# Kernel tuning notes

Measured on AMD Instinct MI355X. Metric: run time of the kernel, lower is better.

The kernel has to match this reference:

```python
import jax, jax.numpy as jnp
import numpy as np

B, N, IN_DIM, D, H, NC = 4, 1024, 8, 128, 8, 64
DK = D // H      # per-head key/value dim = 16
FF = 512         # hard-coded feedforward hidden
N_ENC = 6        # encoder layers


def _u(key, shape):
    s = 1.0 / np.sqrt(shape[-1])
    return jax.random.uniform(key, shape, jnp.float32, -s, s)


def setup_inputs() -> dict:
    key = jax.random.key(0)
    ks = jax.random.split(key, 24)
    inp = {}
    inp["node_inputs"] = jax.random.normal(ks[0], (B, N, IN_DIM), jnp.float32)
    inp["node_padding_mask"] = jnp.zeros((B, 1, N), jnp.int32)
    inp["edge_mask"] = jax.random.randint(ks[1], (B, N, N), 0, 2).astype(jnp.int32)
    inp["center_mask"] = jnp.zeros((B, 1, NC), jnp.int32)
    inp["center_index"] = jax.random.randint(ks[2], (B, 1, NC), 0, N)
    inp["target_index"] = jax.random.randint(ks[3], (B, 1, 1), 0, N)
    inp["current_index"] = jax.random.randint(ks[4], (B, 1, 1), 0, N)
    inp["edge_inputs"] = jax.random.randint(ks[5], (B, N, 20), 0, N)
    # params
    inp["init_W"] = _u(ks[6], (IN_DIM, D)); inp["init_b"] = jnp.zeros((D,), jnp.float32)
    inp["enc_wq"] = _u(ks[7], (N_ENC, H, D, DK))
    inp["enc_wk"] = _u(ks[8], (N_ENC, H, D, DK))
    inp["enc_wv"] = _u(ks[9], (N_ENC, H, D, DK))
    inp["enc_wo"] = _u(ks[10], (N_ENC, H, DK, D))
    inp["enc_ln1_g"] = jnp.ones((N_ENC, D), jnp.float32); inp["enc_ln1_b"] = jnp.zeros((N_ENC, D), jnp.float32)
    inp["enc_w1"] = _u(ks[11], (N_ENC, D, FF)); inp["enc_b1"] = jnp.zeros((N_ENC, FF), jnp.float32)
    inp["enc_w2"] = _u(ks[12], (N_ENC, FF, D)); inp["enc_b2"] = jnp.zeros((N_ENC, D), jnp.float32)
    inp["enc_ln2_g"] = jnp.ones((N_ENC, D), jnp.float32); inp["enc_ln2_b"] = jnp.zeros((N_ENC, D), jnp.float32)
    inp["dec_wq"] = _u(ks[13], (H, D, DK))
    inp["dec_wk"] = _u(ks[14], (H, D, DK))
    inp["dec_wv"] = _u(ks[15], (H, D, DK))
    inp["dec_wo"] = _u(ks[16], (H, DK, D))
    inp["dec_ln1_g"] = jnp.ones((D,), jnp.float32); inp["dec_ln1_b"] = jnp.zeros((D,), jnp.float32)
    inp["dec_w1"] = _u(ks[17], (D, FF)); inp["dec_b1"] = jnp.zeros((FF,), jnp.float32)
    inp["dec_w2"] = _u(ks[18], (FF, D)); inp["dec_b2"] = jnp.zeros((D,), jnp.float32)
    inp["dec_ln2_g"] = jnp.ones((D,), jnp.float32); inp["dec_ln2_b"] = jnp.zeros((D,), jnp.float32)
    inp["tgt_W"] = _u(ks[19], (2 * D, D)); inp["tgt_b"] = jnp.zeros((D,), jnp.float32)
    inp["ptr_wq"] = _u(ks[20], (D, D))
    inp["ptr_wk"] = _u(ks[21], (D, D))
    return inp


def _ln(x, g, b):
    m = jnp.mean(x, -1, keepdims=True)
    v = jnp.mean((x - m) ** 2, -1, keepdims=True)
    return (x - m) * jax.lax.rsqrt(v + 1e-5) * g + b


def _mha(q, k, v, wq, wk, wv, wo, mask):
    # per-head projections exactly as the torch module: [H, B, n, DK]
    Q = jnp.einsum('bqd,hde->hbqe', q, wq)
    K = jnp.einsum('bkd,hde->hbke', k, wk)
    V = jnp.einsum('bkd,hde->hbke', v, wv)
    U = jnp.einsum('hbqe,hbke->hbqk', Q, K) * (1.0 / np.sqrt(DK))
    if mask is not None:
        U = jnp.where(mask[None] > 0, -1e8, U)
    A = jax.nn.softmax(U, axis=-1)
    Hd = jnp.einsum('hbqk,hbke->hbqe', A, V)
    out = jnp.einsum('hbqe,hed->bqd', Hd, wo)
    return out, A


def _gather(x, idx):
    # x [B, N, D], idx [B, M, 1] -> [B, M, D]  (torch.gather with repeat)
    return jnp.take_along_axis(x, jnp.broadcast_to(idx, (x.shape[0], idx.shape[1], x.shape[2])), axis=1)


def reference(node_inputs, node_padding_mask, edge_mask, center_mask, center_index,
              target_index, current_index, edge_inputs,
              init_W, init_b,
              enc_wq, enc_wk, enc_wv, enc_wo, enc_ln1_g, enc_ln1_b,
              enc_w1, enc_b1, enc_w2, enc_b2, enc_ln2_g, enc_ln2_b,
              dec_wq, dec_wk, dec_wv, dec_wo, dec_ln1_g, dec_ln1_b,
              dec_w1, dec_b1, dec_w2, dec_b2, dec_ln2_g, dec_ln2_b,
              tgt_W, tgt_b, ptr_wq, ptr_wk):
    x = node_inputs @ init_W + init_b                      # initial_embedding
    enc_mask = edge_mask + node_padding_mask               # attn_mask + key_padding_mask, [B,N,N]
    for i in range(N_ENC):                                 # Encoder, 6 layers
        h = _ln(x, enc_ln1_g[i], enc_ln1_b[i])
        a, _ = _mha(h, h, h, enc_wq[i], enc_wk[i], enc_wv[i], enc_wo[i], enc_mask)
        h = a + x
        f = _ln(h, enc_ln2_g[i], enc_ln2_b[i])
        f = jax.nn.relu(f @ enc_w1[i] + enc_b1[i]) @ enc_w2[i] + enc_b2[i]
        x = f + h
    enh = x                                                # enhanced_node_feature [B,N,D]
    ci = jnp.transpose(center_index, (0, 2, 1))            # [B,NC,1]
    tgt_f = _gather(enh, target_index)                     # [B,1,D]
    cur_f = _gather(enh, current_index)                    # [B,1,D]
    cen_f = _gather(enh, ci)                               # [B,NC,D]
    # target_decoder (1 DecoderLayer; normalization1 applied to tgt AND memory)
    tgt_n = _ln(tgt_f, dec_ln1_g, dec_ln1_b)
    mem_n = _ln(enh, dec_ln1_g, dec_ln1_b)
    a, _ = _mha(tgt_n, mem_n, mem_n, dec_wq, dec_wk, dec_wv, dec_wo, node_padding_mask)
    h = a + tgt_f
    f = _ln(h, dec_ln2_g, dec_ln2_b)
    f = jax.nn.relu(f @ dec_w1 + dec_b1) @ dec_w2 + dec_b2
    enh_tgt = f + h                                        # [B,1,D]
    emb_tgt = jnp.concatenate([enh_tgt, tgt_f], -1) @ tgt_W + tgt_b
    # pointer1 (SingleHeadAttention, key_dim = D, tanh clipping 10)
    Q = emb_tgt @ ptr_wq                                   # [B,1,D]
    K = cen_f @ ptr_wk                                     # [B,NC,D]
    U = jnp.einsum('bqd,bkd->bqk', Q, K) * (1.0 / np.sqrt(D))
    U = 10.0 * jnp.tanh(U)
    U = jnp.where(center_mask == 1, -1e8, U)
    center_logp = jax.nn.log_softmax(U, axis=-1)[:, 0, :]  # [B,NC]
    idx = jnp.argmax(center_logp, axis=1)
    bidx = jnp.arange(B)
    selected_center_index = ci[bidx, idx, :]               # [B,1]
    selected_center_feature = cen_f[bidx, idx, :][:, None, :]  # [B,1,D]
    return (enh, cur_f, selected_center_index, selected_center_feature, center_logp, cen_f)
```

## Files before the change

kernel.cpp:

```cpp
#include <hip/hip_runtime.h>

constexpr int kB = 4, kN = 1024, kIn = 8, kD = 128, kH = 8, kNC = 64,
              kDK = 16, kFF = 512, kEnc = 6, kR = kB * kN;

__device__ __forceinline__ float wredsum(float v) {
  v += __shfl_xor(v, 1);  v += __shfl_xor(v, 2);  v += __shfl_xor(v, 4);
  v += __shfl_xor(v, 8);  v += __shfl_xor(v, 16); v += __shfl_xor(v, 32);
  return v;
}
__device__ __forceinline__ float wredmax(float v) {
  v = fmaxf(v, __shfl_xor(v, 1));  v = fmaxf(v, __shfl_xor(v, 2));
  v = fmaxf(v, __shfl_xor(v, 4));  v = fmaxf(v, __shfl_xor(v, 8));
  v = fmaxf(v, __shfl_xor(v, 16)); v = fmaxf(v, __shfl_xor(v, 32));
  return v;
}
__device__ __forceinline__ float red4(float v) {
  v += __shfl_xor(v, 1);  v += __shfl_xor(v, 2);
  return v;
}


__global__ __launch_bounds__(256) void repack_qkv(
    const float* __restrict__ wq, const float* __restrict__ wk,
    const float* __restrict__ wv, float* __restrict__ out, int layers) {
  int i = blockIdx.x * 256 + threadIdx.x;
  if (i >= layers * kD * kD) return;
  int l = i / (kD * kD);
  int rem = i - l * kD * kD;
  int d = rem >> 7;
  int c = rem & 127;
  int src = ((l * kH + (c >> 4)) * kD + d) * kDK + (c & 15);
  out[(size_t)(l * 3 + 0) * 16384 + rem] = wq[src];
  out[(size_t)(l * 3 + 1) * 16384 + rem] = wk[src];
  out[(size_t)(l * 3 + 2) * 16384 + rem] = wv[src];
}

__global__ __launch_bounds__(256) void pack_mask(
    const int* __restrict__ edge_mask, const int* __restrict__ pad_mask,
    unsigned long long* __restrict__ bits_t) {
  int row = blockIdx.x;
  int b = row / kN;
  int q = row % kN;
  int lane = threadIdx.x & 63;
  int wv = threadIdx.x >> 6;
  for (int c0 = wv; c0 < 16; c0 += 4) {
    int k = c0 * 64 + lane;
    int m = edge_mask[(size_t)row * kN + k] + pad_mask[b * kN + k];
    unsigned long long bal = __ballot(m > 0);
    if (lane == 0) bits_t[((size_t)b * 16 + c0) * kN + q] = bal;
  }
}

__global__ __launch_bounds__(256) void pack_pad(
    const int* __restrict__ pad_mask, unsigned long long* __restrict__ bits) {
  int b = blockIdx.x;
  int lane = threadIdx.x & 63;
  int wv = threadIdx.x >> 6;
  for (int c0 = wv; c0 < 16; c0 += 4) {
    int k = c0 * 64 + lane;
    unsigned long long bal = __ballot(pad_mask[b * kN + k] > 0);
    if (lane == 0) bits[b * 16 + c0] = bal;
  }
}

__global__ __launch_bounds__(256) void init_proj(
    const float* __restrict__ ni, const float* __restrict__ W,
    const float* __restrict__ bias, float* __restrict__ x) {
  int i = blockIdx.x * 256 + threadIdx.x;
  int r = i >> 7, c = i & 127;
  float acc = bias[c];
#pragma unroll
  for (int k = 0; k < kIn; k++) acc = fmaf(ni[r * kIn + k], W[k * kD + c], acc);
  x[i] = acc;
}

template <int K, int LN, int RELU, int MODE>
__global__ __launch_bounds__(256) void gtile4(
    const float* __restrict__ A, const float* __restrict__ Wg,
    const float* __restrict__ gamma, const float* __restrict__ beta,
    const float* __restrict__ bias, const float* __restrict__ resid,
    float* __restrict__ O0, float* __restrict__ O1, float* __restrict__ O2,
    int Cfull) {
  constexpr int NC = K / 32;
  __shared__ float As[16][K + 4];
  __shared__ float Ws[2][32][128];
  int r0 = blockIdx.x * 16;
  int y = blockIdx.y;
  const float* Wb;
  int wstride;
  if constexpr (MODE == 2) { Wb = Wg + (size_t)y * K * 128; wstride = 128; }
  else { Wb = Wg + (size_t)y * 128; wstride = Cfull; }

  if constexpr (LN) {
    static_assert(K == 128, "LN requires K==128");
    int w = threadIdx.x >> 6, lane = threadIdx.x & 63;
#pragma unroll
    for (int i = 0; i < 4; i++) {
      int rr = w * 4 + i;
      const float* xr = A + (size_t)(r0 + rr) * 128;
      float2 v = *(const float2*)(xr + lane * 2);
      float mean = wredsum(v.x + v.y) * (1.0f / 128.f);
      float dx = v.x - mean, dy = v.y - mean;
      float var = wredsum(dx * dx + dy * dy) * (1.0f / 128.f);
      float rstd = rsqrtf(var + 1e-5f);
      int c = lane * 2;
      As[rr][c] = dx * rstd * gamma[c] + beta[c];
      As[rr][c + 1] = dy * rstd * gamma[c + 1] + beta[c + 1];
    }
  } else {
    constexpr int NF4 = K / 4;
    for (int f = threadIdx.x; f < 16 * NF4; f += 256) {
      int row = f / NF4, c4i = f % NF4;
      *(float4*)&As[row][c4i * 4] =
          *(const float4*)(A + (size_t)(r0 + row) * K + c4i * 4);
    }
  }

  int wrow = threadIdx.x >> 5;
  int wc4 = threadIdx.x & 31;
  float4 wreg[4];
  auto loadW = [&](int kc) {
    const float* Wr = Wb + (size_t)(kc * 32 + wrow) * wstride + wc4 * 4;
#pragma unroll
    for (int j = 0; j < 4; j++)
      wreg[j] = *(const float4*)(Wr + (size_t)8 * j * wstride);
  };
  auto writeW = [&](int buf) {
#pragma unroll
    for (int j = 0; j < 4; j++)
      *(float4*)&Ws[buf][wrow + 8 * j][wc4 * 4] = wreg[j];
  };

  loadW(0);
  writeW(0);

  int c4 = (threadIdx.x & 31) * 4;
  int rg = threadIdx.x >> 5;
  float acc[2][4] = {};
  for (int kc = 0; kc < NC; kc++) {
    if (kc + 1 < NC) loadW(kc + 1);
    __syncthreads();
#pragma unroll
    for (int k4 = 0; k4 < 8; k4++) {
      float4 a0 = *(const float4*)&As[rg * 2][kc * 32 + k4 * 4];
      float4 a1 = *(const float4*)&As[rg * 2 + 1][kc * 32 + k4 * 4];
#pragma unroll
      for (int m = 0; m < 4; m++) {
        float4 wv = *(const float4*)&Ws[kc & 1][k4 * 4 + m][c4];
        float av0 = ((const float*)&a0)[m];
        float av1 = ((const float*)&a1)[m];
        acc[0][0] = fmaf(av0, wv.x, acc[0][0]);
        acc[0][1] = fmaf(av0, wv.y, acc[0][1]);
        acc[0][2] = fmaf(av0, wv.z, acc[0][2]);
        acc[0][3] = fmaf(av0, wv.w, acc[0][3]);
        acc[1][0] = fmaf(av1, wv.x, acc[1][0]);
        acc[1][1] = fmaf(av1, wv.y, acc[1][1]);
        acc[1][2] = fmaf(av1, wv.z, acc[1][2]);
        acc[1][3] = fmaf(av1, wv.w, acc[1][3]);
      }
    }
    if (kc + 1 < NC) writeW((kc + 1) & 1);
  }

#pragma unroll
  for (int rr = 0; rr < 2; rr++) {
    int r = r0 + rg * 2 + rr;
    if constexpr (MODE == 2) {
#pragma unroll
      for (int j = 0; j < 4; j++) {
        int c = c4 + j;
        float v = acc[rr][j];
        int hh = c >> 4, e = c & 15;
        int bb = r >> 10, n = r & 1023;
        float* P = (y == 0) ? O0 : (y == 1) ? O1 : O2;
        P[(((size_t)(bb * kH + hh)) * kN + n) * kDK + e] = v;
      }
    } else {
      int colg = y * 128 + c4;
      float4 v = make_float4(acc[rr][0], acc[rr][1], acc[rr][2], acc[rr][3]);
      if (bias) {
        float4 bv = *(const float4*)(bias + colg);
        v.x += bv.x; v.y += bv.y; v.z += bv.z; v.w += bv.w;
      }
      if (resid) {
        float4 rv = *(const float4*)(resid + (size_t)r * Cfull + colg);
        v.x += rv.x; v.y += rv.y; v.z += rv.z; v.w += rv.w;
      }
      if (RELU) {
        v.x = fmaxf(v.x, 0.f); v.y = fmaxf(v.y, 0.f);
        v.z = fmaxf(v.z, 0.f); v.w = fmaxf(v.w, 0.f);
      }
      *(float4*)(O0 + (size_t)r * Cfull + colg) = v;
    }
  }
}

__global__ __launch_bounds__(512) void attn_flash3(
    const float* __restrict__ Q, const float* __restrict__ K,
    const float* __restrict__ V, const unsigned long long* __restrict__ bits_t,
    float* __restrict__ Hd) {
  __shared__ float Ks[8][64][20];
  __shared__ float Vs[8][64][20];
  int bh = blockIdx.x, qt = blockIdx.y;
  int b = bh >> 3, h = bh & 7;
  int w = threadIdx.x >> 6, lane = threadIdx.x & 63;
  int q0 = qt * 128 + lane, q1 = q0 + 64;
  const float4* qp0 = (const float4*)(Q + ((size_t)bh * kN + q0) * kDK);
  const float4* qp1 = (const float4*)(Q + ((size_t)bh * kN + q1) * kDK);
  float4 qa0 = qp0[0], qa1 = qp0[1], qa2 = qp0[2], qa3 = qp0[3];
  float4 qb0 = qp1[0], qb1 = qp1[1], qb2 = qp1[2], qb3 = qp1[3];
  const float* Kb = K + (size_t)bh * kN * kDK;
  const float* Vb = V + (size_t)bh * kN * kDK;
  float mx0 = -3.0e38f, l0 = 0.f, mx1 = -3.0e38f, l1 = 0.f;
  float acc0[16], acc1[16];
#pragma unroll
  for (int e = 0; e < 16; e++) { acc0[e] = 0.f; acc1[e] = 0.f; }
  for (int t = 0; t < 2; t++) {
    int kk = w * 128 + t * 64 + lane;
    const float4* kp = (const float4*)(Kb + (size_t)kk * kDK);
    float4 ka = kp[0], kb2 = kp[1], kc = kp[2], kd = kp[3];
    const float4* vp = (const float4*)(Vb + (size_t)kk * kDK);
    float4 va = vp[0], vb = vp[1], vc = vp[2], vd = vp[3];
    unsigned long long mb0 = bits_t[((size_t)b * 16 + w * 2 + t) * kN + q0];
    unsigned long long mb1 = bits_t[((size_t)b * 16 + w * 2 + t) * kN + q1];
    ((float4*)&Ks[w][lane][0])[0] = ka;  ((float4*)&Ks[w][lane][0])[1] = kb2;
    ((float4*)&Ks[w][lane][0])[2] = kc;  ((float4*)&Ks[w][lane][0])[3] = kd;
    ((float4*)&Vs[w][lane][0])[0] = va;  ((float4*)&Vs[w][lane][0])[1] = vb;
    ((float4*)&Vs[w][lane][0])[2] = vc;  ((float4*)&Vs[w][lane][0])[3] = vd;
#pragma unroll 2
    for (int k2 = 0; k2 < 64; k2++) {
      const float4* kr = (const float4*)&Ks[w][k2][0];
      float4 k0 = kr[0], k1 = kr[1], k2v = kr[2], k3 = kr[3];
      float s0 = qa0.x * k0.x + qa0.y * k0.y + qa0.z * k0.z + qa0.w * k0.w
               + qa1.x * k1.x + qa1.y * k1.y + qa1.z * k1.z + qa1.w * k1.w
               + qa2.x * k2v.x + qa2.y * k2v.y + qa2.z * k2v.z + qa2.w * k2v.w
               + qa3.x * k3.x + qa3.y * k3.y + qa3.z * k3.z + qa3.w * k3.w;
      float s1 = qb0.x * k0.x + qb0.y * k0.y + qb0.z * k0.z + qb0.w * k0.w
               + qb1.x * k1.x + qb1.y * k1.y + qb1.z * k1.z + qb1.w * k1.w
               + qb2.x * k2v.x + qb2.y * k2v.y + qb2.z * k2v.z + qb2.w * k2v.w
               + qb3.x * k3.x + qb3.y * k3.y + qb3.z * k3.z + qb3.w * k3.w;
      s0 *= 0.25f; s1 *= 0.25f;
      if ((mb0 >> k2) & 1ull) s0 = -1e8f;
      if ((mb1 >> k2) & 1ull) s1 = -1e8f;
      float d0 = s0 - mx0;
      if (d0 > 8.f) {
        float sc = __expf(-d0);
        l0 *= sc;
#pragma unroll
        for (int e = 0; e < 16; e++) acc0[e] *= sc;
        mx0 = s0; d0 = 0.f;
      }
      float p0 = __expf(d0);
      l0 += p0;
      float d1 = s1 - mx1;
      if (d1 > 8.f) {
        float sc = __expf(-d1);
        l1 *= sc;
#pragma unroll
        for (int e = 0; e < 16; e++) acc1[e] *= sc;
        mx1 = s1; d1 = 0.f;
      }
      float p1 = __expf(d1);
      l1 += p1;
      const float4* vr = (const float4*)&Vs[w][k2][0];
      float4 v0 = vr[0], v1 = vr[1], v2 = vr[2], v3 = vr[3];
      acc0[0] = fmaf(p0, v0.x, acc0[0]);   acc0[1] = fmaf(p0, v0.y, acc0[1]);
      acc0[2] = fmaf(p0, v0.z, acc0[2]);   acc0[3] = fmaf(p0, v0.w, acc0[3]);
      acc0[4] = fmaf(p0, v1.x, acc0[4]);   acc0[5] = fmaf(p0, v1.y, acc0[5]);
      acc0[6] = fmaf(p0, v1.z, acc0[6]);   acc0[7] = fmaf(p0, v1.w, acc0[7]);
      acc0[8] = fmaf(p0, v2.x, acc0[8]);   acc0[9] = fmaf(p0, v2.y, acc0[9]);
      acc0[10] = fmaf(p0, v2.z, acc0[10]); acc0[11] = fmaf(p0, v2.w, acc0[11]);
      acc0[12] = fmaf(p0, v3.x, acc0[12]); acc0[13] = fmaf(p0, v3.y, acc0[13]);
      acc0[14] = fmaf(p0, v3.z, acc0[14]); acc0[15] = fmaf(p0, v3.w, acc0[15]);
      acc1[0] = fmaf(p1, v0.x, acc1[0]);   acc1[1] = fmaf(p1, v0.y, acc1[1]);
      acc1[2] = fmaf(p1, v0.z, acc1[2]);   acc1[3] = fmaf(p1, v0.w, acc1[3]);
      acc1[4] = fmaf(p1, v1.x, acc1[4]);   acc1[5] = fmaf(p1, v1.y, acc1[5]);
      acc1[6] = fmaf(p1, v1.z, acc1[6]);   acc1[7] = fmaf(p1, v1.w, acc1[7]);
      acc1[8] = fmaf(p1, v2.x, acc1[8]);   acc1[9] = fmaf(p1, v2.y, acc1[9]);
      acc1[10] = fmaf(p1, v2.z, acc1[10]); acc1[11] = fmaf(p1, v2.w, acc1[11]);
      acc1[12] = fmaf(p1, v3.x, acc1[12]); acc1[13] = fmaf(p1, v3.y, acc1[13]);
      acc1[14] = fmaf(p1, v3.z, acc1[14]); acc1[15] = fmaf(p1, v3.w, acc1[15]);
    }
  }
  __syncthreads();
  float* M0 = &Ks[w][lane][0];
  float* M1 = &Vs[w][lane][0];
#pragma unroll
  for (int e = 0; e < 16; e++) { M0[e] = acc0[e]; M1[e] = acc1[e]; }
  M0[16] = mx0; M0[17] = l0;
  M1[16] = mx1; M1[17] = l1;
  __syncthreads();
#pragma unroll
  for (int half = 0; half < 2; half++) {
    const float* M = half ? &Vs[0][0][0] : &Ks[0][0][0];
    float mv[8];
#pragma unroll
    for (int p = 0; p < 8; p++) mv[p] = M[(p * 64 + lane) * 20 + 16];
    float mstar = mv[0];
#pragma unroll
    for (int p = 1; p < 8; p++) mstar = fmaxf(mstar, mv[p]);
    float f[8];
    float L = 0.f;
#pragma unroll
    for (int p = 0; p < 8; p++) {
      f[p] = __expf(mv[p] - mstar);
      L += f[p] * M[(p * 64 + lane) * 20 + 17];
    }
    float invL = 1.0f / L;
    float o[2];
#pragma unroll
    for (int e = 0; e < 2; e++) {
      int ei = w * 2 + e;
      float a = 0.f;
#pragma unroll
      for (int p = 0; p < 8; p++) a += f[p] * M[(p * 64 + lane) * 20 + ei];
      o[e] = a * invL;
    }
    int q = qt * 128 + half * 64 + lane;
    *(float2*)(Hd + ((size_t)(b * kN + q)) * kD + h * kDK + w * 2) =
        make_float2(o[0], o[1]);
  }
}


__global__ __launch_bounds__(256) void dec_prep(
    const float* __restrict__ enh, const int* __restrict__ tgt_idx,
    const int* __restrict__ cur_idx, const int* __restrict__ cen_idx,
    const float* __restrict__ Wq,
    const float* __restrict__ ln1_g, const float* __restrict__ ln1_b,
    const float* __restrict__ dec_wk,
    float* __restrict__ out_curf, float* __restrict__ out_cenf,
    float* __restrict__ tgtf_ws, float* __restrict__ qk_ws) {
  __shared__ float tgtf_s[128], tgtn[128], qd[128];
  int b = blockIdx.x, t = threadIdx.x;
  int lane = t & 63, w = t >> 6;
  int ti = tgt_idx[b], cui = cur_idx[b];
  if (t < 128) {
    float tf = enh[((size_t)b * kN + ti) * kD + t];
    tgtf_s[t] = tf;
    tgtf_ws[b * kD + t] = tf;
    out_curf[b * kD + t] = enh[((size_t)b * kN + cui) * kD + t];
  }
  for (int i = t; i < kNC * kD; i += 256) {
    int c = i >> 7, e = i & 127;
    out_cenf[((size_t)b * kNC + c) * kD + e] =
        enh[((size_t)b * kN + cen_idx[b * kNC + c]) * kD + e];
  }
  __syncthreads();
  if (w == 0) {
    float vx = tgtf_s[lane * 2], vy = tgtf_s[lane * 2 + 1];
    float mean = wredsum(vx + vy) * (1.0f / 128.f);
    float dx = vx - mean, dy = vy - mean;
    float var = wredsum(dx * dx + dy * dy) * (1.0f / 128.f);
    float rstd = rsqrtf(var + 1e-5f);
    tgtn[lane * 2] = dx * rstd * ln1_g[lane * 2] + ln1_b[lane * 2];
    tgtn[lane * 2 + 1] = dy * rstd * ln1_g[lane * 2 + 1] + ln1_b[lane * 2 + 1];
  }
  __syncthreads();
  if (t < 128) {
    float a = 0.f;
#pragma unroll 8
    for (int k = 0; k < 128; k++) a = fmaf(tgtn[k], Wq[k * 128 + t], a);
    qd[t] = a;
  }
  __syncthreads();
  int h = t >> 5, d0 = (t & 31) * 4;
#pragma unroll
  for (int j = 0; j < 4; j++) {
    int d = d0 + j;
    const float4* wp = (const float4*)(dec_wk + (((size_t)h * 128 + d) << 4));
    float a = 0.f;
#pragma unroll
    for (int r = 0; r < 4; r++) {
      float4 wv = wp[r];
      a += wv.x * qd[h * 16 + r * 4] + wv.y * qd[h * 16 + r * 4 + 1] +
           wv.z * qd[h * 16 + r * 4 + 2] + wv.w * qd[h * 16 + r * 4 + 3];
    }
    qk_ws[b * 1024 + h * 128 + d] = 0.25f * a;
  }
}

__global__ __launch_bounds__(256) void dec_score(
    const float* __restrict__ enh, const float* __restrict__ ln_g,
    const float* __restrict__ ln_b, const float* __restrict__ qk_ws,
    const unsigned long long* __restrict__ padbits,
    float* __restrict__ ln_ws, float* __restrict__ scores) {
  __shared__ float qs[8][128];
  int b = blockIdx.x, nt = blockIdx.y, t = threadIdx.x;
  for (int i = t; i < 1024; i += 256) ((float*)qs)[i] = qk_ws[b * 1024 + i];
  __syncthreads();
  int w = t >> 6, lane = t & 63, ri = lane >> 2, q4 = lane & 3;
  int n = nt * 64 + w * 16 + ri;
  const float* row = enh + ((size_t)b * kN + n) * kD;
  float4 xv[8];
#pragma unroll
  for (int j = 0; j < 8; j++) xv[j] = *(const float4*)(row + j * 16 + q4 * 4);
  float s1 = 0.f;
#pragma unroll
  for (int j = 0; j < 8; j++) s1 += xv[j].x + xv[j].y + xv[j].z + xv[j].w;
  s1 = red4(s1);
  float mean = s1 * (1.0f / 128.f);
  float s2 = 0.f;
#pragma unroll
  for (int j = 0; j < 8; j++) {
    xv[j].x -= mean; xv[j].y -= mean; xv[j].z -= mean; xv[j].w -= mean;
    s2 += xv[j].x * xv[j].x + xv[j].y * xv[j].y + xv[j].z * xv[j].z +
          xv[j].w * xv[j].w;
  }
  s2 = red4(s2);
  float rstd = rsqrtf(s2 * (1.0f / 128.f) + 1e-5f);
#pragma unroll
  for (int j = 0; j < 8; j++) {
    int d0 = j * 16 + q4 * 4;
    float4 g = *(const float4*)(ln_g + d0);
    float4 be = *(const float4*)(ln_b + d0);
    xv[j].x = xv[j].x * rstd * g.x + be.x;
    xv[j].y = xv[j].y * rstd * g.y + be.y;
    xv[j].z = xv[j].z * rstd * g.z + be.z;
    xv[j].w = xv[j].w * rstd * g.w + be.w;
    *(float4*)(ln_ws + ((size_t)b * kN + n) * kD + d0) = xv[j];
  }
  bool mk = (padbits[b * 16 + (n >> 6)] >> (n & 63)) & 1ull;
#pragma unroll
  for (int h = 0; h < 8; h++) {
    float p = 0.f;
#pragma unroll
    for (int j = 0; j < 8; j++) {
      float4 qv = *(const float4*)&qs[h][j * 16 + q4 * 4];
      p += xv[j].x * qv.x + xv[j].y * qv.y + xv[j].z * qv.z + xv[j].w * qv.w;
    }
    p = red4(p);
    if (q4 == 0) scores[((size_t)b * 8 + h) * 1024 + n] = mk ? -1e8f : p;
  }
}

__global__ __launch_bounds__(256) void dec_softmax(
    const float* __restrict__ scores, float* __restrict__ ml) {
  int b = blockIdx.x, t = threadIdx.x, w = t >> 6, lane = t & 63;
  for (int hi = 0; hi < 2; hi++) {
    int h = w + hi * 4;
    const float* sr = scores + ((size_t)b * 8 + h) * 1024;
    float v[16];
    float m = -3.0e38f;
#pragma unroll
    for (int i = 0; i < 16; i++) { v[i] = sr[i * 64 + lane]; m = fmaxf(m, v[i]); }
    m = wredmax(m);
    float l = 0.f;
#pragma unroll
    for (int i = 0; i < 16; i++) l += __expf(v[i] - m);
    l = wredsum(l);
    if (lane == 0) { ml[(b * 8 + h) * 2] = m; ml[(b * 8 + h) * 2 + 1] = l; }
  }
}

__global__ __launch_bounds__(256) void dec_attnsum(
    const float* __restrict__ ln_ws, const float* __restrict__ scores,
    const float* __restrict__ ml, float* __restrict__ partial) {
  __shared__ float lns[64][128];
  __shared__ float ps[8][64];
  int b = blockIdx.x, nt = blockIdx.y, t = threadIdx.x;
  for (int i = t; i < 64 * 32; i += 256) {
    int nn = i >> 5, c4 = i & 31;
    *(float4*)&lns[nn][c4 * 4] =
        *(const float4*)(ln_ws + ((size_t)b * kN + nt * 64 + nn) * kD + c4 * 4);
  }
  for (int i = t; i < 512; i += 256) {
    int h = i >> 6, nn = i & 63;
    float m = ml[(b * 8 + h) * 2], l = ml[(b * 8 + h) * 2 + 1];
    ps[h][nn] =
        __expf(scores[((size_t)b * 8 + h) * 1024 + nt * 64 + nn] - m) / l;
  }
  __syncthreads();
  int h = t >> 5, d0 = (t & 31) * 4;
  float4 acc = make_float4(0.f, 0.f, 0.f, 0.f);
  for (int nn = 0; nn < 64; nn++) {
    float p = ps[h][nn];
    float4 lv = *(const float4*)&lns[nn][d0];
    acc.x = fmaf(p, lv.x, acc.x); acc.y = fmaf(p, lv.y, acc.y);
    acc.z = fmaf(p, lv.z, acc.z); acc.w = fmaf(p, lv.w, acc.w);
  }
  *(float4*)(partial + ((size_t)(b * 16 + nt) * 8 + h) * 128 + d0) = acc;
}

__global__ __launch_bounds__(1024) void dec_tail(
    const float* __restrict__ partial, const float* __restrict__ dec_wv,
    const float* __restrict__ dwo, const float* __restrict__ tgtf_ws,
    const float* __restrict__ cenf_g, const float* __restrict__ Kp,
    const int* __restrict__ cen_idx, const int* __restrict__ center_mask,
    const float* __restrict__ ln2_g, const float* __restrict__ ln2_b,
    const float* __restrict__ w1, const float* __restrict__ b1,
    const float* __restrict__ w2, const float* __restrict__ b2,
    const float* __restrict__ tgt_W, const float* __restrict__ tgt_b,
    const float* __restrict__ ptr_wq,
    float* __restrict__ out_selidx, float* __restrict__ out_selfeat,
    float* __restrict__ out_logp) {
  __shared__ float wsum[8][132];
  __shared__ float red[8][132];
  __shared__ float red2[2][520];
  __shared__ float red16[16][68];
  __shared__ float tgtf[128], hdd[128], dechs[128], decfs[128], dects[512],
                   embs[128], qps[128];
  __shared__ int bi_s;
  int b = blockIdx.x, t = threadIdx.x;
  int c = t & 127, p = t >> 7;
  int lane = t & 63, w = t >> 6;

  {
    float a = 0.f;
#pragma unroll
    for (int tt = 0; tt < 16; tt++)
      a += partial[((size_t)(b * 16 + tt) * 8 + p) * 128 + c];
    wsum[p][c] = a;
    if (t < 128) tgtf[t] = tgtf_ws[b * kD + t];
  }
  __syncthreads();

  {
    int h = c >> 4, e = c & 15;
    float a = 0.f;
#pragma unroll
    for (int i = 0; i < 16; i++) {
      int d = p * 16 + i;
      a = fmaf(wsum[h][d], dec_wv[((size_t)h * 128 + d) * 16 + e], a);
    }
    red[p][c] = a;
  }
  __syncthreads();
  if (t < 128) {
    float a = 0.f;
#pragma unroll
    for (int q = 0; q < 8; q++) a += red[q][t];
    hdd[t] = a;
  }
  __syncthreads();

  {
    float a = 0.f;
#pragma unroll
    for (int i = 0; i < 16; i++) {
      int k = p * 16 + i;
      a = fmaf(hdd[k], dwo[k * 128 + c], a);
    }
    red[p][c] = a;
  }
  __syncthreads();
  if (t < 128) {
    float a = 0.f;
#pragma unroll
    for (int q = 0; q < 8; q++) a += red[q][t];
    dechs[t] = a + tgtf[t];
  }
  __syncthreads();

  if (w == 0) {
    float vx = dechs[lane * 2], vy = dechs[lane * 2 + 1];
    float mean = wredsum(vx + vy) * (1.0f / 128.f);
    float dx = vx - mean, dy = vy - mean;
    float var = wredsum(dx * dx + dy * dy) * (1.0f / 128.f);
    float rstd = rsqrtf(var + 1e-5f);
    decfs[lane * 2] = dx * rstd * ln2_g[lane * 2] + ln2_b[lane * 2];
    decfs[lane * 2 + 1] = dy * rstd * ln2_g[lane * 2 + 1] + ln2_b[lane * 2 + 1];
  }
  __syncthreads();

  {
    int c5 = t & 511, p2 = t >> 9;
    float a = 0.f;
#pragma unroll 8
    for (int i = 0; i < 64; i++) {
      int k = p2 * 64 + i;
      a = fmaf(decfs[k], w1[k * 512 + c5], a);
    }
    red2[p2][c5] = a;
  }
  __syncthreads();
  if (t < 512) dects[t] = fmaxf(red2[0][t] + red2[1][t] + b1[t], 0.f);
  __syncthreads();

  {
    float a = 0.f;
#pragma unroll 8
    for (int i = 0; i < 64; i++) {
      int k = p * 64 + i;
      a = fmaf(dects[k], w2[k * 128 + c], a);
    }
    red[p][c] = a;
  }
  __syncthreads();
  if (t < 128) {
    float a = 0.f;
#pragma unroll
    for (int q = 0; q < 8; q++) a += red[q][t];
    decfs[t] = a + b2[t] + dechs[t];
  }
  __syncthreads();

  {
    float a = 0.f;
#pragma unroll
    for (int i = 0; i < 32; i++) {
      int k = p * 32 + i;
      float vkk = (k < 128) ? decfs[k] : tgtf[k - 128];
      a = fmaf(vkk, tgt_W[k * 128 + c], a);
    }
    red[p][c] = a;
  }
  __syncthreads();
  if (t < 128) {
    float a = 0.f;
#pragma unroll
    for (int q = 0; q < 8; q++) a += red[q][t];
    embs[t] = a + tgt_b[t];
  }
  __syncthreads();

  {
    float a = 0.f;
#pragma unroll
    for (int i = 0; i < 16; i++) {
      int k = p * 16 + i;
      a = fmaf(embs[k], ptr_wq[k * 128 + c], a);
    }
    red[p][c] = a;
  }
  __syncthreads();
  if (t < 128) {
    float a = 0.f;
#pragma unroll
    for (int q = 0; q < 8; q++) a += red[q][t];
    qps[t] = a;
  }
  __syncthreads();

  {
    int cen = t & 63, p16 = t >> 6;
    float a = 0.f;
#pragma unroll
    for (int i = 0; i < 8; i++) {
      int k = p16 * 8 + i;
      a = fmaf(qps[k], Kp[((size_t)(b * kNC + cen)) * kD + k], a);
    }
    red16[p16][cen] = a;
  }
  __syncthreads();
  if (w == 0) {
    float u = 0.f;
#pragma unroll
    for (int q = 0; q < 16; q++) u += red16[q][lane];
    u *= 0.08838834764831845f;
    u = 10.0f * tanhf(u);
    if (center_mask[b * kNC + lane] == 1) u = -1e8f;
    float m = wredmax(u);
    float ex = __expf(u - m);
    float sum = wredsum(ex);
    out_logp[b * kNC + lane] = u - m - logf(sum);
    float bm = u; int bi = lane;
#pragma unroll
    for (int o = 32; o; o >>= 1) {
      float om = __shfl_xor(bm, o);
      int oi = __shfl_xor(bi, o);
      if (om > bm || (om == bm && oi < bi)) { bm = om; bi = oi; }
    }
    if (lane == 0) {
      out_selidx[b] = (float)cen_idx[b * kNC + bi];
      bi_s = bi;
    }
  }
  __syncthreads();
  if (t < 128)
    out_selfeat[b * kD + t] = cenf_g[((size_t)(b * kNC + bi_s)) * kD + t];
}


extern "C" void kernel_launch(void* const* d_in, const int* in_sizes, int n_in,
                              void* d_out, int out_size, void* d_ws,
                              size_t ws_size, hipStream_t stream) {
  (void)in_sizes; (void)n_in; (void)out_size; (void)ws_size;
  const float* node_inputs = (const float*)d_in[0];
  const int* pad_mask = (const int*)d_in[1];
  const int* edge_mask = (const int*)d_in[2];
  const int* center_mask = (const int*)d_in[3];
  const int* center_index = (const int*)d_in[4];
  const int* target_index = (const int*)d_in[5];
  const int* current_index = (const int*)d_in[6];
  const float* init_W = (const float*)d_in[8];
  const float* init_b = (const float*)d_in[9];
  const float* enc_wq = (const float*)d_in[10];
  const float* enc_wk = (const float*)d_in[11];
  const float* enc_wv = (const float*)d_in[12];
  const float* enc_wo = (const float*)d_in[13];
  const float* enc_ln1_g = (const float*)d_in[14];
  const float* enc_ln1_b = (const float*)d_in[15];
  const float* enc_w1 = (const float*)d_in[16];
  const float* enc_b1 = (const float*)d_in[17];
  const float* enc_w2 = (const float*)d_in[18];
  const float* enc_b2 = (const float*)d_in[19];
  const float* enc_ln2_g = (const float*)d_in[20];
  const float* enc_ln2_b = (const float*)d_in[21];
  const float* dec_wq = (const float*)d_in[22];
  const float* dec_wk = (const float*)d_in[23];
  const float* dec_wv = (const float*)d_in[24];
  const float* dec_wo = (const float*)d_in[25];
  const float* dec_ln1_g = (const float*)d_in[26];
  const float* dec_ln1_b = (const float*)d_in[27];
  const float* dec_w1 = (const float*)d_in[28];
  const float* dec_b1 = (const float*)d_in[29];
  const float* dec_w2 = (const float*)d_in[30];
  const float* dec_b2 = (const float*)d_in[31];
  const float* dec_ln2_g = (const float*)d_in[32];
  const float* dec_ln2_b = (const float*)d_in[33];
  const float* tgt_W = (const float*)d_in[34];
  const float* tgt_b = (const float*)d_in[35];
  const float* ptr_wq = (const float*)d_in[36];
  const float* ptr_wk = (const float*)d_in[37];

  float* out_enh = (float*)d_out;
  float* out_curf = out_enh + kB * kN * kD;
  float* out_selidx = out_curf + kB * kD;
  float* out_selfeat = out_selidx + kB;
  float* out_logp = out_selfeat + kB * kD;
  float* out_cenf = out_logp + kB * kNC;

  char* wsp = (char*)d_ws;
  size_t off = 0;
  auto alloc = [&](size_t n) {
    char* p = wsp + off;
    off = (off + n + 255) & ~(size_t)255;
    return p;
  };
  float* x   = (float*)alloc(kR * kD * 4);
  float* h2  = (float*)alloc(kR * kD * 4);
  float* Qb  = (float*)alloc(kR * kD * 4);
  float* Kb  = (float*)alloc(kR * kD * 4);
  float* Vb  = (float*)alloc(kR * kD * 4);
  float* Hd  = (float*)alloc(kR * kD * 4);
  float* tb  = (float*)alloc(kR * kFF * 4);
  unsigned long long* bits_t  = (unsigned long long*)alloc(kR * 16 * 8);
  unsigned long long* padbits = (unsigned long long*)alloc(kB * 16 * 8);
  float* ewqkv = (float*)alloc(kEnc * 3 * kD * kD * 4);
  float* dqkvW = (float*)alloc(3 * kD * kD * 4);
  float* ln_ws = (float*)alloc(kR * kD * 4);
  float* scores_ws = (float*)alloc(kB * kH * kN * 4);
  float* ml_ws = (float*)alloc(kB * kH * 2 * 4);
  float* partial_ws = (float*)alloc(kB * 16 * kH * kD * 4);
  float* qk_ws = (float*)alloc(kB * kH * kD * 4);
  float* tgtf_ws = (float*)alloc(kB * kD * 4);
  float* Kp_ws = (float*)alloc(kB * kNC * kD * 4);

  repack_qkv<<<(kEnc * kD * kD + 255) / 256, 256, 0, stream>>>(
      enc_wq, enc_wk, enc_wv, ewqkv, kEnc);
  repack_qkv<<<(kD * kD + 255) / 256, 256, 0, stream>>>(
      dec_wq, dec_wk, dec_wv, dqkvW, 1);
  pack_mask<<<kB * kN, 256, 0, stream>>>(edge_mask, pad_mask, bits_t);
  pack_pad<<<kB, 256, 0, stream>>>(pad_mask, padbits);
  init_proj<<<kR * kD / 256, 256, 0, stream>>>(node_inputs, init_W, init_b, x);

  for (int l = 0; l < kEnc; l++) {
    const float* wo_l = enc_wo + (size_t)l * kH * kDK * kD;
    gtile4<128, 1, 0, 2><<<dim3(kR / 16, 3), 256, 0, stream>>>(
        x, ewqkv + (size_t)l * 3 * kD * kD, enc_ln1_g + l * kD,
        enc_ln1_b + l * kD, nullptr, nullptr, Qb, Kb, Vb, kD);
    attn_flash3<<<dim3(kB * kH, kN / 128), 512, 0, stream>>>(Qb, Kb, Vb,
                                                             bits_t, Hd);
    gtile4<128, 0, 0, 0><<<dim3(kR / 16, 1), 256, 0, stream>>>(
        Hd, wo_l, nullptr, nullptr, nullptr, x, h2, nullptr, nullptr, kD);
    gtile4<128, 1, 1, 0><<<dim3(kR / 16, kFF / 128), 256, 0, stream>>>(
        h2, enc_w1 + (size_t)l * kD * kFF, enc_ln2_g + l * kD,
        enc_ln2_b + l * kD, enc_b1 + l * kFF, nullptr, tb, nullptr, nullptr, kFF);
    float* xout = (l == kEnc - 1) ? out_enh : x;
    gtile4<512, 0, 0, 0><<<dim3(kR / 16, 1), 256, 0, stream>>>(
        tb, enc_w2 + (size_t)l * kFF * kD, nullptr, nullptr, enc_b2 + l * kD,
        h2, xout, nullptr, nullptr, kD);
  }

  dec_prep<<<kB, 256, 0, stream>>>(out_enh, target_index, current_index,
                                   center_index, dqkvW, dec_ln1_g, dec_ln1_b,
                                   dec_wk, out_curf, out_cenf, tgtf_ws, qk_ws);
  gtile4<128, 0, 0, 0><<<dim3(kB * kNC / 16, 1), 256, 0, stream>>>(
      out_cenf, ptr_wk, nullptr, nullptr, nullptr, nullptr, Kp_ws, nullptr,
      nullptr, kD);
  dec_score<<<dim3(kB, 16), 256, 0, stream>>>(out_enh, dec_ln1_g, dec_ln1_b,
                                              qk_ws, padbits, ln_ws, scores_ws);
  dec_softmax<<<kB, 256, 0, stream>>>(scores_ws, ml_ws);
  dec_attnsum<<<dim3(kB, 16), 256, 0, stream>>>(ln_ws, scores_ws, ml_ws,
                                                partial_ws);
  dec_tail<<<kB, 1024, 0, stream>>>(
      partial_ws, dec_wv, dec_wo, tgtf_ws, out_cenf, Kp_ws, center_index,
      center_mask, dec_ln2_g, dec_ln2_b, dec_w1, dec_b1, dec_w2, dec_b2,
      tgt_W, tgt_b, ptr_wq, out_selidx, out_selfeat, out_logp);
}
```

Before: 797.9 us.

## Split encoder attention over key halves with four queries per thread and merge

Replaces the single-pass flash attention kernel with a split-K version. Each block handles 256 queries against one half of the keys, and each thread keeps four queries in registers so every K/V row read from shared memory is reused four times. Partial max, sum and accumulators go to a workspace, and a separate merge kernel combines the two halves. This raises per-thread register pressure, adds a global round trip for partials plus an extra launch per layer, and serializes the intra-block reduction over four syncs.

```diff
diff --git a/kernel.cpp b/kernel.cpp
--- a/kernel.cpp
+++ b/kernel.cpp
@@ -195,131 +195,141 @@
   }
 }
 
-__global__ __launch_bounds__(512) void attn_flash3(
+__global__ __launch_bounds__(512) void attn_part(
     const float* __restrict__ Q, const float* __restrict__ K,
     const float* __restrict__ V, const unsigned long long* __restrict__ bits_t,
-    float* __restrict__ Hd) {
+    float* __restrict__ part) {
   __shared__ float Ks[8][64][20];
   __shared__ float Vs[8][64][20];
-  int bh = blockIdx.x, qt = blockIdx.y;
+  int bh = blockIdx.x, qt = blockIdx.y, ks = blockIdx.z;
+  int b = bh >> 3;
+  int w = threadIdx.x >> 6, lane = threadIdx.x & 63;
+  int qbase = qt * 256 + lane;
+  float4 qr[4][4];
+#pragma unroll
+  for (int i = 0; i < 4; i++) {
+    const float4* qp = (const float4*)(Q + ((size_t)bh * kN + qbase + i * 64) * kDK);
+    qr[i][0] = qp[0]; qr[i][1] = qp[1]; qr[i][2] = qp[2]; qr[i][3] = qp[3];
+  }
+  int kk = ks * 512 + w * 64 + lane;
+  {
+    const float4* kp = (const float4*)(K + ((size_t)bh * kN + kk) * kDK);
+    const float4* vp = (const float4*)(V + ((size_t)bh * kN + kk) * kDK);
+    ((float4*)&Ks[w][lane][0])[0] = kp[0]; ((float4*)&Ks[w][lane][0])[1] = kp[1];
+    ((float4*)&Ks[w][lane][0])[2] = kp[2]; ((float4*)&Ks[w][lane][0])[3] = kp[3];
+    ((float4*)&Vs[w][lane][0])[0] = vp[0]; ((float4*)&Vs[w][lane][0])[1] = vp[1];
+    ((float4*)&Vs[w][lane][0])[2] = vp[2]; ((float4*)&Vs[w][lane][0])[3] = vp[3];
+  }
+  int tile = ks * 8 + w;
+  unsigned long long mb[4];
+#pragma unroll
+  for (int i = 0; i < 4; i++)
+    mb[i] = bits_t[((size_t)b * 16 + tile) * kN + qbase + i * 64];
+
+  float mx[4], lsum[4], acc[4][16];
+#pragma unroll
+  for (int i = 0; i < 4; i++) {
+    mx[i] = -3.0e38f; lsum[i] = 0.f;
+#pragma unroll
+    for (int e = 0; e < 16; e++) acc[i][e] = 0.f;
+  }
+
+#pragma unroll 2
+  for (int k2 = 0; k2 < 64; k2++) {
+    const float4* kr = (const float4*)&Ks[w][k2][0];
+    float4 k0 = kr[0], k1 = kr[1], k2v = kr[2], k3 = kr[3];
+    const float4* vr = (const float4*)&Vs[w][k2][0];
+    float4 v0 = vr[0], v1 = vr[1], v2 = vr[2], v3 = vr[3];
+#pragma unroll
+    for (int i = 0; i < 4; i++) {
+      float s = qr[i][0].x * k0.x + qr[i][0].y * k0.y + qr[i][0].z * k0.z +
+                qr[i][0].w * k0.w + qr[i][1].x * k1.x + qr[i][1].y * k1.y +
+                qr[i][1].z * k1.z + qr[i][1].w * k1.w + qr[i][2].x * k2v.x +
+                qr[i][2].y * k2v.y + qr[i][2].z * k2v.z + qr[i][2].w * k2v.w +
+                qr[i][3].x * k3.x + qr[i][3].y * k3.y + qr[i][3].z * k3.z +
+                qr[i][3].w * k3.w;
+      s *= 0.25f;
+      if ((mb[i] >> k2) & 1ull) s = -1e8f;
+      float d = s - mx[i];
+      if (d > 8.f) {
+        float sc = __expf(-d);
+        lsum[i] *= sc;
+#pragma unroll
+        for (int e = 0; e < 16; e++) acc[i][e] *= sc;
+        mx[i] = s; d = 0.f;
+      }
+      float p = __expf(d);
+      lsum[i] += p;
+      acc[i][0] = fmaf(p, v0.x, acc[i][0]);
+      acc[i][1] = fmaf(p, v0.y, acc[i][1]);
+      acc[i][2] = fmaf(p, v0.z, acc[i][2]);
+      acc[i][3] = fmaf(p, v0.w, acc[i][3]);
+      acc[i][4] = fmaf(p, v1.x, acc[i][4]);
+      acc[i][5] = fmaf(p, v1.y, acc[i][5]);
+      acc[i][6] = fmaf(p, v1.z, acc[i][6]);
+      acc[i][7] = fmaf(p, v1.w, acc[i][7]);
+      acc[i][8] = fmaf(p, v2.x, acc[i][8]);
+      acc[i][9] = fmaf(p, v2.y, acc[i][9]);
+      acc[i][10] = fmaf(p, v2.z, acc[i][10]);
+      acc[i][11] = fmaf(p, v2.w, acc[i][11]);
+      acc[i][12] = fmaf(p, v3.x, acc[i][12]);
+      acc[i][13] = fmaf(p, v3.y, acc[i][13]);
+      acc[i][14] = fmaf(p, v3.z, acc[i][14]);
+      acc[i][15] = fmaf(p, v3.w, acc[i][15]);
+    }
+  }
+  __syncthreads();
+  for (int i = 0; i < 4; i++) {
+    float* dst = &Ks[w][lane][0];
+#pragma unroll
+    for (int e = 0; e < 16; e++) dst[e] = acc[i][e];
+    dst[16] = mx[i];
+    dst[17] = lsum[i];
+    __syncthreads();
+    if (w == 0) {
+      float mv[8];
+#pragma unroll
+      for (int p = 0; p < 8; p++) mv[p] = Ks[p][lane][16];
+      float mstar = mv[0];
+#pragma unroll
+      for (int p = 1; p < 8; p++) mstar = fmaxf(mstar, mv[p]);
+      float f[8];
+      float L = 0.f;
+#pragma unroll
+      for (int p = 0; p < 8; p++) {
+        f[p] = __expf(mv[p] - mstar);
+        L += f[p] * Ks[p][lane][17];
+      }
+      int q = qt * 256 + i * 64 + lane;
+      float* op = part + ((size_t)(ks * 32 + bh) * kN + q) * 20;
+#pragma unroll
+      for (int e = 0; e < 16; e++) {
+        float a = 0.f;
+#pragma unroll
+        for (int p = 0; p < 8; p++) a += f[p] * Ks[p][lane][e];
+        op[e] = a;
+      }
+      op[16] = mstar;
+      op[17] = L;
+    }
+    __syncthreads();
+  }
+}
+
+__global__ __launch_bounds__(256) void attn_merge(
+    const float* __restrict__ part, float* __restrict__ Hd) {
+  int idx = blockIdx.x * 256 + threadIdx.x;
+  int bh = idx >> 10, q = idx & 1023;
   int b = bh >> 3, h = bh & 7;
-  int w = threadIdx.x >> 6, lane = threadIdx.x & 63;
-  int q0 = qt * 128 + lane, q1 = q0 + 64;
-  const float4* qp0 = (const float4*)(Q + ((size_t)bh * kN + q0) * kDK);
-  const float4* qp1 = (const float4*)(Q + ((size_t)bh * kN + q1) * kDK);
-  float4 qa0 = qp0[0], qa1 = qp0[1], qa2 = qp0[2], qa3 = qp0[3];
-  float4 qb0 = qp1[0], qb1 = qp1[1], qb2 = qp1[2], qb3 = qp1[3];
-  const float* Kb = K + (size_t)bh * kN * kDK;
-  const float* Vb = V + (size_t)bh * kN * kDK;
-  float mx0 = -3.0e38f, l0 = 0.f, mx1 = -3.0e38f, l1 = 0.f;
-  float acc0[16], acc1[16];
-#pragma unroll
-  for (int e = 0; e < 16; e++) { acc0[e] = 0.f; acc1[e] = 0.f; }
-  for (int t = 0; t < 2; t++) {
-    int kk = w * 128 + t * 64 + lane;
-    const float4* kp = (const float4*)(Kb + (size_t)kk * kDK);
-    float4 ka = kp[0], kb2 = kp[1], kc = kp[2], kd = kp[3];
-    const float4* vp = (const float4*)(Vb + (size_t)kk * kDK);
-    float4 va = vp[0], vb = vp[1], vc = vp[2], vd = vp[3];
-    unsigned long long mb0 = bits_t[((size_t)b * 16 + w * 2 + t) * kN + q0];
-    unsigned long long mb1 = bits_t[((size_t)b * 16 + w * 2 + t) * kN + q1];
-    ((float4*)&Ks[w][lane][0])[0] = ka;  ((float4*)&Ks[w][lane][0])[1] = kb2;
-    ((float4*)&Ks[w][lane][0])[2] = kc;  ((float4*)&Ks[w][lane][0])[3] = kd;
-    ((float4*)&Vs[w][lane][0])[0] = va;  ((float4*)&Vs[w][lane][0])[1] = vb;
-    ((float4*)&Vs[w][lane][0])[2] = vc;  ((float4*)&Vs[w][lane][0])[3] = vd;
-#pragma unroll 2
-    for (int k2 = 0; k2 < 64; k2++) {
-      const float4* kr = (const float4*)&Ks[w][k2][0];
-      float4 k0 = kr[0], k1 = kr[1], k2v = kr[2], k3 = kr[3];
-      float s0 = qa0.x * k0.x + qa0.y * k0.y + qa0.z * k0.z + qa0.w * k0.w
-               + qa1.x * k1.x + qa1.y * k1.y + qa1.z * k1.z + qa1.w * k1.w
-               + qa2.x * k2v.x + qa2.y * k2v.y + qa2.z * k2v.z + qa2.w * k2v.w
-               + qa3.x * k3.x + qa3.y * k3.y + qa3.z * k3.z + qa3.w * k3.w;
-      float s1 = qb0.x * k0.x + qb0.y * k0.y + qb0.z * k0.z + qb0.w * k0.w
-               + qb1.x * k1.x + qb1.y * k1.y + qb1.z * k1.z + qb1.w * k1.w
-               + qb2.x * k2v.x + qb2.y * k2v.y + qb2.z * k2v.z + qb2.w * k2v.w
-               + qb3.x * k3.x + qb3.y * k3.y + qb3.z * k3.z + qb3.w * k3.w;
-      s0 *= 0.25f; s1 *= 0.25f;
-      if ((mb0 >> k2) & 1ull) s0 = -1e8f;
-      if ((mb1 >> k2) & 1ull) s1 = -1e8f;
-      float d0 = s0 - mx0;
-      if (d0 > 8.f) {
-        float sc = __expf(-d0);
-        l0 *= sc;
-#pragma unroll
-        for (int e = 0; e < 16; e++) acc0[e] *= sc;
-        mx0 = s0; d0 = 0.f;
-      }
-      float p0 = __expf(d0);
-      l0 += p0;
-      float d1 = s1 - mx1;
-      if (d1 > 8.f) {
-        float sc = __expf(-d1);
-        l1 *= sc;
-#pragma unroll
-        for (int e = 0; e < 16; e++) acc1[e] *= sc;
-        mx1 = s1; d1 = 0.f;
-      }
-      float p1 = __expf(d1);
-      l1 += p1;
-      const float4* vr = (const float4*)&Vs[w][k2][0];
-      float4 v0 = vr[0], v1 = vr[1], v2 = vr[2], v3 = vr[3];
-      acc0[0] = fmaf(p0, v0.x, acc0[0]);   acc0[1] = fmaf(p0, v0.y, acc0[1]);
-      acc0[2] = fmaf(p0, v0.z, acc0[2]);   acc0[3] = fmaf(p0, v0.w, acc0[3]);
-      acc0[4] = fmaf(p0, v1.x, acc0[4]);   acc0[5] = fmaf(p0, v1.y, acc0[5]);
-      acc0[6] = fmaf(p0, v1.z, acc0[6]);   acc0[7] = fmaf(p0, v1.w, acc0[7]);
-      acc0[8] = fmaf(p0, v2.x, acc0[8]);   acc0[9] = fmaf(p0, v2.y, acc0[9]);
-      acc0[10] = fmaf(p0, v2.z, acc0[10]); acc0[11] = fmaf(p0, v2.w, acc0[11]);
-      acc0[12] = fmaf(p0, v3.x, acc0[12]); acc0[13] = fmaf(p0, v3.y, acc0[13]);
-      acc0[14] = fmaf(p0, v3.z, acc0[14]); acc0[15] = fmaf(p0, v3.w, acc0[15]);
-      acc1[0] = fmaf(p1, v0.x, acc1[0]);   acc1[1] = fmaf(p1, v0.y, acc1[1]);
-      acc1[2] = fmaf(p1, v0.z, acc1[2]);   acc1[3] = fmaf(p1, v0.w, acc1[3]);
-      acc1[4] = fmaf(p1, v1.x, acc1[4]);   acc1[5] = fmaf(p1, v1.y, acc1[5]);
-      acc1[6] = fmaf(p1, v1.z, acc1[6]);   acc1[7] = fmaf(p1, v1.w, acc1[7]);
-      acc1[8] = fmaf(p1, v2.x, acc1[8]);   acc1[9] = fmaf(p1, v2.y, acc1[9]);
-      acc1[10] = fmaf(p1, v2.z, acc1[10]); acc1[11] = fmaf(p1, v2.w, acc1[11]);
-      acc1[12] = fmaf(p1, v3.x, acc1[12]); acc1[13] = fmaf(p1, v3.y, acc1[13]);
-      acc1[14] = fmaf(p1, v3.z, acc1[14]); acc1[15] = fmaf(p1, v3.w, acc1[15]);
-    }
-  }
-  __syncthreads();
-  float* M0 = &Ks[w][lane][0];
-  float* M1 = &Vs[w][lane][0];
-#pragma unroll
-  for (int e = 0; e < 16; e++) { M0[e] = acc0[e]; M1[e] = acc1[e]; }
-  M0[16] = mx0; M0[17] = l0;
-  M1[16] = mx1; M1[17] = l1;
-  __syncthreads();
-#pragma unroll
-  for (int half = 0; half < 2; half++) {
-    const float* M = half ? &Vs[0][0][0] : &Ks[0][0][0];
-    float mv[8];
-#pragma unroll
-    for (int p = 0; p < 8; p++) mv[p] = M[(p * 64 + lane) * 20 + 16];
-    float mstar = mv[0];
-#pragma unroll
-    for (int p = 1; p < 8; p++) mstar = fmaxf(mstar, mv[p]);
-    float f[8];
-    float L = 0.f;
-#pragma unroll
-    for (int p = 0; p < 8; p++) {
-      f[p] = __expf(mv[p] - mstar);
-      L += f[p] * M[(p * 64 + lane) * 20 + 17];
-    }
-    float invL = 1.0f / L;
-    float o[2];
-#pragma unroll
-    for (int e = 0; e < 2; e++) {
-      int ei = w * 2 + e;
-      float a = 0.f;
-#pragma unroll
-      for (int p = 0; p < 8; p++) a += f[p] * M[(p * 64 + lane) * 20 + ei];
-      o[e] = a * invL;
-    }
-    int q = qt * 128 + half * 64 + lane;
-    *(float2*)(Hd + ((size_t)(b * kN + q)) * kD + h * kDK + w * 2) =
-        make_float2(o[0], o[1]);
-  }
+  const float* p0 = part + ((size_t)(0 * 32 + bh) * kN + q) * 20;
+  const float* p1 = part + ((size_t)(1 * 32 + bh) * kN + q) * 20;
+  float m0 = p0[16], l0 = p0[17], m1 = p1[16], l1 = p1[17];
+  float ms = fmaxf(m0, m1);
+  float f0 = __expf(m0 - ms), f1 = __expf(m1 - ms);
+  float inv = 1.0f / (f0 * l0 + f1 * l1);
+  float* op = Hd + ((size_t)(b * kN + q)) * kD + h * kDK;
+#pragma unroll
+  for (int e = 0; e < 16; e++) op[e] = (f0 * p0[e] + f1 * p1[e]) * inv;
 }
 
 
@@ -746,6 +756,7 @@
   float* qk_ws = (float*)alloc(kB * kH * kD * 4);
   float* tgtf_ws = (float*)alloc(kB * kD * 4);
   float* Kp_ws = (float*)alloc(kB * kNC * kD * 4);
+  float* apart_ws = (float*)alloc((size_t)2 * 32 * kN * 20 * 4);
 
   repack_qkv<<<(kEnc * kD * kD + 255) / 256, 256, 0, stream>>>(
       enc_wq, enc_wk, enc_wv, ewqkv, kEnc);
@@ -760,8 +771,9 @@
     gtile4<128, 1, 0, 2><<<dim3(kR / 16, 3), 256, 0, stream>>>(
         x, ewqkv + (size_t)l * 3 * kD * kD, enc_ln1_g + l * kD,
         enc_ln1_b + l * kD, nullptr, nullptr, Qb, Kb, Vb, kD);
-    attn_flash3<<<dim3(kB * kH, kN / 128), 512, 0, stream>>>(Qb, Kb, Vb,
-                                                             bits_t, Hd);
+    attn_part<<<dim3(kB * kH, kN / 256, 2), 512, 0, stream>>>(Qb, Kb, Vb,
+                                                              bits_t, apart_ws);
+    attn_merge<<<(kB * kH * kN) / 256, 256, 0, stream>>>(apart_ws, Hd);
     gtile4<128, 0, 0, 0><<<dim3(kR / 16, 1), 256, 0, stream>>>(
         Hd, wo_l, nullptr, nullptr, nullptr, x, h2, nullptr, nullptr, kD);
     gtile4<128, 1, 1, 0><<<dim3(kR / 16, kFF / 128), 256, 0, stream>>>(
```

Measured after the change: 824.6 us. +3.3%, slower.
